# Kernel optimization log

Measured on AMD Instinct MI355X. Metric: run time of the kernel, lower is better.

The kernel has to match this reference:

```python
import jax, jax.numpy as jnp
import numpy as np

N_HEAD = 8
HIDDEN = 512
EPS_LN = 1e-3  # keras LayerNormalization default epsilon


def layernorm(x, gamma, beta, eps=EPS_LN):
    mu = jnp.mean(x, axis=-1, keepdims=True)
    var = jnp.mean((x - mu) ** 2, axis=-1, keepdims=True)
    return (x - mu) * jax.lax.rsqrt(var + eps) * gamma + beta


def setup_inputs() -> dict:
    key = jax.random.key(0)
    ks = jax.random.split(key, 10)
    bs, NE, F = 512, 128, HIDDEN
    x = jax.random.normal(ks[0], (bs, NE, F), dtype=jnp.float32)
    mask = (jax.random.uniform(ks[1], (bs, 1, NE)) < 0.85).astype(jnp.float32)
    # guarantee at least one live entity per row
    mask = mask.at[:, :, 0].set(1.0)
    s = 1.0 / np.sqrt(F)
    Wqk = jax.random.normal(ks[2], (F, 2 * HIDDEN), dtype=jnp.float32) * s
    bqk = jnp.zeros((2 * HIDDEN,), jnp.float32)
    Wv = jax.random.normal(ks[3], (F, HIDDEN), dtype=jnp.float32) * s
    bv = jnp.zeros((HIDDEN,), jnp.float32)
    Wmlp = jax.random.normal(ks[4], (F, HIDDEN), dtype=jnp.float32) * s
    bmlp = jnp.zeros((HIDDEN,), jnp.float32)
    g_pre = jnp.ones((F,), jnp.float32)
    b_pre = jnp.zeros((F,), jnp.float32)
    g_post = jnp.ones((F,), jnp.float32)
    b_post = jnp.zeros((F,), jnp.float32)
    return dict(x=x, mask=mask, Wqk=Wqk, bqk=bqk, Wv=Wv, bv=bv,
                Wmlp=Wmlp, bmlp=bmlp, g_pre=g_pre, b_pre=b_pre,
                g_post=g_post, b_post=b_post)


def reference(x, mask, Wqk, bqk, Wv, bv, Wmlp, bmlp, g_pre, b_pre, g_post, b_post):
    bs, NE, F = x.shape
    h, d = N_HEAD, HIDDEN // N_HEAD
    x4 = x[:, None]  # (bs, 1, NE, F)

    # pre-norm only feeds qkv projections; residual uses raw x4
    inp = layernorm(x4, g_pre, b_pre)

    qk = (inp @ Wqk + bqk).reshape(bs, 1, NE, h, d, 2)
    q, k = qk[..., 0], qk[..., 1]                       # (bs,1,NE,h,d)
    v = (inp @ Wv + bv).reshape(bs, 1, NE, h, d)

    logits = jnp.einsum('btnhd,btmhd->bthnm', q, k) / np.sqrt(d)  # (bs,1,h,NE,NE)

    m5 = mask[:, :, None, None, :]                      # (bs,1,1,1,NE)
    logits = logits - (1.0 - m5) * 1e10
    logits = logits - jnp.max(logits, axis=-1, keepdims=True)
    un = jnp.exp(logits) * m5
    p = un / (jnp.sum(un, axis=-1, keepdims=True) + 1e-10)
    p = p * m5

    att = jnp.einsum('bthnm,btmhd->btnhd', p, v).reshape(bs, 1, NE, HIDDEN)
    a = att @ Wmlp + bmlp                               # mlp_layer=1, no activation
    y = x4 + a                                          # residual
    y = layernorm(y, g_post, b_post)

    # masked average pooling over entities
    mE = mask[..., None]                                # (bs,1,NE,1)
    pooled = jnp.sum(y * mE, axis=-2) / (jnp.sum(mE, axis=-2) + 1e-5)  # (bs,1,F)
    return pooled.reshape(bs, F)
```

## Files before the change

### kernel.cpp

```cpp
#include <hip/hip_runtime.h>
#include <hip/hip_bf16.h>


typedef __bf16 bf16;
typedef __bf16 bf16x8 __attribute__((ext_vector_type(8)));
typedef __bf16 bf16x4 __attribute__((ext_vector_type(4)));
typedef float f32x4 __attribute__((ext_vector_type(4)));

__device__ __forceinline__ f32x4 mfma16(bf16x8 a, bf16x8 b, f32x4 c) {
    return __builtin_amdgcn_mfma_f32_16x16x32_bf16(a, b, c, 0, 0, 0);
}

typedef const unsigned int __attribute__((address_space(1)))* gptr_t;
typedef unsigned int __attribute__((address_space(3)))* lptr_t;
__device__ __forceinline__ void gld16(const void* g, void* l) {
    __builtin_amdgcn_global_load_lds((gptr_t)g, (lptr_t)l, 16, 0, 0);
}

#define SWZ(byteoff, row) ((byteoff) ^ (((row) & 7) << 4))


__global__ __launch_bounds__(256) void prep_split_kernel(
    const float* __restrict__ Wqk, const float* __restrict__ bqk,
    const float* __restrict__ Wv, const float* __restrict__ bv,
    const float* __restrict__ Wmlp,
    bf16* __restrict__ Wqkv_s, bf16* __restrict__ Wmlp_t, float* __restrict__ bQKV)
{
    int t = blockIdx.x * 256 + threadIdx.x;
    if (t < 524288) {
        int k = t >> 10, c = t & 1023;
        int h = c >> 7, w7 = c & 127, d = w7 >> 1, isK = w7 & 1;
        int n = isK * 512 + h * 64 + d;
        int tn = n >> 7, nc = n & 127, kc = k >> 6, kw = k & 63;
        Wqkv_s[((size_t)(tn * 8 + kc) * 128 + nc) * 64 + kw] = (bf16)Wqk[t];
    } else if (t < 786432) {
        int u = t - 524288;
        int k = u >> 9, c = u & 511;
        int n = 1024 + c;
        int tn = n >> 7, nc = n & 127, kc = k >> 6, kw = k & 63;
        Wqkv_s[((size_t)(tn * 8 + kc) * 128 + nc) * 64 + kw] = (bf16)Wv[u];
    } else if (t < 1048576) {
        int u = t - 786432;
        int k = u >> 9, c = u & 511;
        int tn = c >> 7, nc = c & 127, kc = k >> 6, kw = k & 63;
        Wmlp_t[((size_t)(tn * 8 + kc) * 128 + nc) * 64 + kw] = (bf16)Wmlp[u];
    } else if (t < 1050112) {
        int j = t - 1048576;
        int region = j >> 9, w9 = j & 511, h = w9 >> 6, d = w9 & 63;
        float v;
        if (region == 0)      v = bqk[h * 128 + d * 2];
        else if (region == 1) v = bqk[h * 128 + d * 2 + 1];
        else                  v = bv[h * 64 + d];
        bQKV[j] = v;
    }
}

__global__ __launch_bounds__(256) void ln_kernel(
    const float* __restrict__ x, const float* __restrict__ g,
    const float* __restrict__ b, bf16* __restrict__ inp)
{
    int row = blockIdx.x * 4 + (threadIdx.x >> 6);
    int lane = threadIdx.x & 63;
    int k0 = lane * 8;
    const float* xr = x + (size_t)row * 512 + k0;
    f32x4 a0 = *(const f32x4*)xr;
    f32x4 a1 = *(const f32x4*)(xr + 4);
    float s = 0.f, ss = 0.f;
#pragma unroll
    for (int i = 0; i < 4; i++) {
        s += a0[i] + a1[i];
        ss += a0[i] * a0[i] + a1[i] * a1[i];
    }
#pragma unroll
    for (int m = 1; m < 64; m <<= 1) {
        s  += __shfl_xor(s, m, 64);
        ss += __shfl_xor(ss, m, 64);
    }
    float mu = s * (1.f / 512.f);
    float rstd = rsqrtf(ss * (1.f / 512.f) - mu * mu + 1e-3f);
    f32x4 g0 = *(const f32x4*)(g + k0);
    f32x4 g1 = *(const f32x4*)(g + k0 + 4);
    f32x4 b0 = *(const f32x4*)(b + k0);
    f32x4 b1 = *(const f32x4*)(b + k0 + 4);
    bf16x8 ov;
#pragma unroll
    for (int i = 0; i < 4; i++) {
        ov[i]     = (bf16)((a0[i] - mu) * rstd * g0[i] + b0[i]);
        ov[i + 4] = (bf16)((a1[i] - mu) * rstd * g1[i] + b1[i]);
    }
    *(bf16x8*)(inp + (size_t)row * 512 + k0) = ov;
}

__global__ __launch_bounds__(256) void qkv_gemm_kernel(
    const bf16* __restrict__ inp, const bf16* __restrict__ Wqkv_s,
    const float* __restrict__ bQKV,
    bf16* __restrict__ q, bf16* __restrict__ kbuf, bf16* __restrict__ vt)
{
    __shared__ __align__(16) bf16 As[128 * 64];
    __shared__ __align__(16) bf16 Bs[128 * 64];
    const int bid = blockIdx.x;
    const int idx = (bid & 7) * 768 + (bid >> 3);
    const int tm = idx / 12, tn = idx % 12;
    const int tid = threadIdx.x;
    const int w = tid >> 6, l = tid & 63;
    const int wr = w >> 1, wc = w & 1;
    const int l15 = l & 15, l4 = l >> 4;

    const f32x4 fz = {0.f, 0.f, 0.f, 0.f};
    f32x4 acc[4][4];
#pragma unroll
    for (int m = 0; m < 4; m++)
#pragma unroll
        for (int n = 0; n < 4; n++) acc[m][n] = fz;

    const int arow = l >> 3;
    const int axc = ((l & 7) ^ arow) * 8;
    const bf16* Abase = inp + (size_t)(tm * 128) * 512;
    const int rsw = (l15 & 7) << 4;

    for (int kc = 0; kc < 8; kc++) {
#pragma unroll
        for (int i = 0; i < 4; i++) {
            int rg = (i * 4 + w) * 8;
            gld16(Abase + (size_t)(rg + arow) * 512 + kc * 64 + axc,
                  As + (i * 4 + w) * 512);
        }
        const bf16* Bbase = Wqkv_s + (size_t)(tn * 8 + kc) * 8192;
#pragma unroll
        for (int i = 0; i < 4; i++) {
            gld16(Bbase + (size_t)((i * 4 + w) * 8 + arow) * 64 + axc,
                  Bs + (i * 4 + w) * 512);
        }
        __syncthreads();
#pragma unroll
        for (int kk = 0; kk < 2; kk++) {
            const int kb = (kk * 64 + l4 * 16) ^ rsw;
            bf16x8 af[4], bfr[4];
#pragma unroll
            for (int m = 0; m < 4; m++)
                af[m] = *(const bf16x8*)((const char*)As + (wr * 64 + m * 16 + l15) * 128 + kb);
#pragma unroll
            for (int n = 0; n < 4; n++)
                bfr[n] = *(const bf16x8*)((const char*)Bs + (wc * 64 + n * 16 + l15) * 128 + kb);
#pragma unroll
            for (int m = 0; m < 4; m++)
#pragma unroll
                for (int n = 0; n < 4; n++)
                    acc[m][n] = mfma16(af[m], bfr[n], acc[m][n]);
        }
        __syncthreads();
    }

    const int colBase = tn * 128 + wc * 64;
    const int mrowBase = tm * 128 + wr * 64;
#pragma unroll
    for (int n = 0; n < 4; n++) {
        int col = colBase + n * 16 + l15;
        float bias = bQKV[col];
        int within = col & 511, hh = within >> 6, dd = within & 63;
#pragma unroll
        for (int m = 0; m < 4; m++) {
            int mr0 = mrowBase + m * 16 + l4 * 4;
            int bb = mr0 >> 7, e0 = mr0 & 127;
            size_t base = (size_t)(bb * 8 + hh) * 8192;
            if (tn < 4) {
#pragma unroll
                for (int r = 0; r < 4; r++)
                    q[base + (size_t)(e0 + r) * 64 + dd] = (bf16)(acc[m][n][r] + bias);
            } else if (tn < 8) {
#pragma unroll
                for (int r = 0; r < 4; r++) {
                    int e = e0 + r;
                    kbuf[base + (size_t)e * 64 + (dd ^ ((e & 7) << 3))] = (bf16)(acc[m][n][r] + bias);
                }
            } else {
                bf16x4 pk;
#pragma unroll
                for (int r = 0; r < 4; r++) pk[r] = (bf16)(acc[m][n][r] + bias);
                *(bf16x4*)(vt + base + (size_t)dd * 128 + (e0 ^ ((dd & 7) << 3))) = pk;
            }
        }
    }
}

__global__ __launch_bounds__(512) void attn_split_kernel(
    const bf16* __restrict__ q, const bf16* __restrict__ kbuf,
    const bf16* __restrict__ vt, const float* __restrict__ mask,
    bf16* __restrict__ att)
{
    __shared__ __align__(16) char Ks[128 * 128];
    __shared__ __align__(16) char VTs[64 * 256];
    __shared__ __align__(16) char Ps[128 * 256];
    __shared__ float mrow[128];

    const int bid = blockIdx.x;
    const int b = bid & 511, h = bid >> 9;
    const size_t bh = (size_t)(b * 8 + h);
    const int tid = threadIdx.x;
    const int w = tid >> 6, l = tid & 63;
    const int l15 = l & 15, l4 = l >> 4, R0 = w * 16;

    const bf16* kb = kbuf + bh * 8192;
    const bf16* vb = vt + bh * 8192;
#pragma unroll
    for (int i = 0; i < 2; i++) {
        gld16(kb + ((i * 8 + w) * 64 + l) * 8, (bf16*)Ks + (i * 8 + w) * 512);
        gld16(vb + ((i * 8 + w) * 64 + l) * 8, (bf16*)VTs + (i * 8 + w) * 512);
    }
    if (tid < 128) mrow[tid] = mask[b * 128 + tid];
    __syncthreads();

    const f32x4 fz = {0.f, 0.f, 0.f, 0.f};
    const bf16* qp = q + bh * 8192 + (size_t)(R0 + l15) * 64 + l4 * 8;
    bf16x8 af0 = *(const bf16x8*)(qp);
    bf16x8 af1 = *(const bf16x8*)(qp + 32);
    f32x4 accL[8];
#pragma unroll
    for (int n = 0; n < 8; n++) accL[n] = fz;
#pragma unroll
    for (int ks = 0; ks < 2; ks++) {
        bf16x8 af = ks ? af1 : af0;
        int k2 = (ks * 32 + l4 * 8) * 2;
#pragma unroll
        for (int nt = 0; nt < 8; nt++) {
            int krow = nt * 16 + l15;
            bf16x8 bfr = *(const bf16x8*)(Ks + krow * 128 + (k2 ^ ((krow & 7) << 4)));
            accL[nt] = mfma16(af, bfr, accL[nt]);
        }
    }
    float pv[32];
#pragma unroll
    for (int r = 0; r < 4; r++) {
        float mx = -1e30f;
#pragma unroll
        for (int nt = 0; nt < 8; nt++) {
            int colk = nt * 16 + l15;
            float v = accL[nt][r] * 0.125f - (1.0f - mrow[colk]) * 1e10f;
            pv[nt * 4 + r] = v;
            mx = fmaxf(mx, v);
        }
#pragma unroll
        for (int m = 1; m < 16; m <<= 1) mx = fmaxf(mx, __shfl_xor(mx, m, 64));
        float sum = 0.f;
#pragma unroll
        for (int nt = 0; nt < 8; nt++) {
            int colk = nt * 16 + l15;
            float e = __expf(pv[nt * 4 + r] - mx) * mrow[colk];
            pv[nt * 4 + r] = e;
            sum += e;
        }
#pragma unroll
        for (int m = 1; m < 16; m <<= 1) sum += __shfl_xor(sum, m, 64);
        float inv = 1.0f / (sum + 1e-10f);
        int prow = R0 + l4 * 4 + r;
#pragma unroll
        for (int nt = 0; nt < 8; nt++) {
            bf16 pb = (bf16)(pv[nt * 4 + r] * inv);
            *(bf16*)(Ps + prow * 256 + SWZ((nt * 16 + l15) * 2, prow)) = pb;
        }
    }
    __syncthreads();

    f32x4 accO[4];
#pragma unroll
    for (int n = 0; n < 4; n++) accO[n] = fz;
#pragma unroll
    for (int ks = 0; ks < 4; ks++) {
        int k2 = (ks * 32 + l4 * 8) * 2;
        int prow = R0 + l15;
        bf16x8 af = *(const bf16x8*)(Ps + prow * 256 + (k2 ^ ((prow & 7) << 4)));
#pragma unroll
        for (int nt = 0; nt < 4; nt++) {
            int d = nt * 16 + l15;
            bf16x8 bfr = *(const bf16x8*)(VTs + d * 256 + (k2 ^ ((d & 7) << 4)));
            accO[nt] = mfma16(af, bfr, accO[nt]);
        }
    }
    bf16* outp = att + (size_t)(b * 128) * 512 + h * 64;
#pragma unroll
    for (int nt = 0; nt < 4; nt++) {
        int d = nt * 16 + l15;
#pragma unroll
        for (int r = 0; r < 4; r++) {
            int e = R0 + l4 * 4 + r;
            outp[(size_t)e * 512 + d] = (bf16)accO[nt][r];
        }
    }
}

__global__ __launch_bounds__(256) void mlp_gemm_kernel(
    const bf16* __restrict__ att, const bf16* __restrict__ Wmlp_t,
    const float* __restrict__ bmlp, float* __restrict__ y)
{
    __shared__ __align__(16) bf16 As[128 * 64];
    __shared__ __align__(16) bf16 Bs[128 * 64];
    const int bid = blockIdx.x;
    const int idx = (bid & 7) * 256 + (bid >> 3);
    const int tm = idx >> 2, tn = idx & 3;
    const int tid = threadIdx.x;
    const int w = tid >> 6, l = tid & 63;
    const int wr = w >> 1, wc = w & 1;
    const int l15 = l & 15, l4 = l >> 4;

    const f32x4 fz = {0.f, 0.f, 0.f, 0.f};
    f32x4 acc[4][4];
#pragma unroll
    for (int m = 0; m < 4; m++)
#pragma unroll
        for (int n = 0; n < 4; n++) acc[m][n] = fz;

    const int arow = l >> 3;
    const int axc = ((l & 7) ^ arow) * 8;
    const bf16* Abase = att + (size_t)(tm * 128) * 512;
    const int rsw = (l15 & 7) << 4;

    for (int kc = 0; kc < 8; kc++) {
#pragma unroll
        for (int i = 0; i < 4; i++) {
            int rg = (i * 4 + w) * 8;
            gld16(Abase + (size_t)(rg + arow) * 512 + kc * 64 + axc,
                  As + (i * 4 + w) * 512);
        }
        const bf16* Bbase = Wmlp_t + (size_t)(tn * 8 + kc) * 8192;
#pragma unroll
        for (int i = 0; i < 4; i++) {
            gld16(Bbase + (size_t)((i * 4 + w) * 8 + arow) * 64 + axc,
                  Bs + (i * 4 + w) * 512);
        }
        __syncthreads();
#pragma unroll
        for (int kk = 0; kk < 2; kk++) {
            const int kb = (kk * 64 + l4 * 16) ^ rsw;
            bf16x8 af[4], bfr[4];
#pragma unroll
            for (int m = 0; m < 4; m++)
                af[m] = *(const bf16x8*)((const char*)As + (wr * 64 + m * 16 + l15) * 128 + kb);
#pragma unroll
            for (int n = 0; n < 4; n++)
                bfr[n] = *(const bf16x8*)((const char*)Bs + (wc * 64 + n * 16 + l15) * 128 + kb);
#pragma unroll
            for (int m = 0; m < 4; m++)
#pragma unroll
                for (int n = 0; n < 4; n++)
                    acc[m][n] = mfma16(af[m], bfr[n], acc[m][n]);
        }
        __syncthreads();
    }

    const int colBase = tn * 128 + wc * 64;
    const int mrowBase = tm * 128 + wr * 64;
#pragma unroll
    for (int n = 0; n < 4; n++) {
        int col = colBase + n * 16 + l15;
        float bias = bmlp[col];
#pragma unroll
        for (int m = 0; m < 4; m++) {
            int row0 = mrowBase + m * 16 + l4 * 4;
#pragma unroll
            for (int r = 0; r < 4; r++)
                y[(size_t)(row0 + r) * 512 + col] = acc[m][n][r] + bias;
        }
    }
}

__global__ __launch_bounds__(512) void pool_kernel(
    const float* __restrict__ y, const float* __restrict__ x,
    const float* __restrict__ mask, const float* __restrict__ gpost,
    const float* __restrict__ bpost, float* __restrict__ out)
{
    __shared__ float partial[8][512];
    __shared__ float mrow[128];
    __shared__ float msum_s;

    const int b = blockIdx.x;
    const int tid = threadIdx.x;
    const int w = tid >> 6, l = tid & 63;
    const int k0 = l * 8;

    if (tid < 128) mrow[tid] = mask[b * 128 + tid];
    __syncthreads();
    if (w == 0) {
        float v = mrow[l] + mrow[64 + l];
#pragma unroll
        for (int m = 1; m < 64; m <<= 1) v += __shfl_xor(v, m, 64);
        if (l == 0) msum_s = v;
    }

    f32x4 g0 = *(const f32x4*)(gpost + k0);
    f32x4 g1 = *(const f32x4*)(gpost + k0 + 4);
    f32x4 b0 = *(const f32x4*)(bpost + k0);
    f32x4 b1 = *(const f32x4*)(bpost + k0 + 4);

    f32x4 a0 = {0.f, 0.f, 0.f, 0.f}, a1 = {0.f, 0.f, 0.f, 0.f};
    for (int i = 0; i < 16; i++) {
        int row = w * 16 + i;
        const float* yr = y + ((size_t)(b * 128 + row)) * 512 + k0;
        const float* xr = x + ((size_t)(b * 128 + row)) * 512 + k0;
        f32x4 v0 = *(const f32x4*)yr + *(const f32x4*)xr;
        f32x4 v1 = *(const f32x4*)(yr + 4) + *(const f32x4*)(xr + 4);
        float s = 0.f, ss = 0.f;
#pragma unroll
        for (int j = 0; j < 4; j++) {
            s += v0[j] + v1[j];
            ss += v0[j] * v0[j] + v1[j] * v1[j];
        }
#pragma unroll
        for (int m = 1; m < 64; m <<= 1) {
            s  += __shfl_xor(s, m, 64);
            ss += __shfl_xor(ss, m, 64);
        }
        float mu = s * (1.f / 512.f);
        float rstd = rsqrtf(ss * (1.f / 512.f) - mu * mu + 1e-3f);
        float mr = mrow[row];
#pragma unroll
        for (int j = 0; j < 4; j++) {
            a0[j] += ((v0[j] - mu) * rstd * g0[j] + b0[j]) * mr;
            a1[j] += ((v1[j] - mu) * rstd * g1[j] + b1[j]) * mr;
        }
    }
#pragma unroll
    for (int j = 0; j < 4; j++) {
        partial[w][k0 + j]     = a0[j];
        partial[w][k0 + 4 + j] = a1[j];
    }
    __syncthreads();
    float t = 0.f;
#pragma unroll
    for (int ww = 0; ww < 8; ww++) t += partial[ww][tid];
    out[(size_t)b * 512 + tid] = t / (msum_s + 1e-5f);
}

__global__ __launch_bounds__(256) void prep_kernel(
    const float* __restrict__ Wqk, const float* __restrict__ bqk,
    const float* __restrict__ Wv, const float* __restrict__ bv,
    const float* __restrict__ Wmlp,
    bf16* __restrict__ Wqkv_t, bf16* __restrict__ Wmlp_t, float* __restrict__ bQKV)
{
    int t = blockIdx.x * 256 + threadIdx.x;
    const int NQKV = 8 * 192 * 512;
    if (t < NQKV) {
        int h = t / (192 * 512);
        int rem = t - h * (192 * 512);
        int n = rem >> 9;
        int k = rem & 511;
        float v;
        if (n < 64)       v = Wqk[k * 1024 + h * 128 + n * 2];
        else if (n < 128) v = Wqk[k * 1024 + h * 128 + (n - 64) * 2 + 1];
        else              v = Wv[k * 512 + h * 64 + (n - 128)];
        Wqkv_t[t] = (bf16)v;
    } else {
        int u = t - NQKV;
        if (u < 512 * 512) {
            int col = u >> 9, k = u & 511;
            Wmlp_t[u] = (bf16)Wmlp[k * 512 + col];
        } else {
            int j = u - 512 * 512;
            if (j < 1536) {
                int h = j / 192, n = j - h * 192;
                float v;
                if (n < 64)       v = bqk[h * 128 + n * 2];
                else if (n < 128) v = bqk[h * 128 + (n - 64) * 2 + 1];
                else              v = bv[h * 64 + (n - 128)];
                bQKV[j] = v;
            }
        }
    }
}

__global__ __launch_bounds__(512) void attn_kernel(
    const bf16* __restrict__ inp, const float* __restrict__ mask,
    const bf16* __restrict__ Wqkv_t, const float* __restrict__ bQKV,
    bf16* __restrict__ att)
{
    __shared__ __align__(16) char Qs[128 * 128];
    __shared__ __align__(16) char Ks[128 * 128];
    __shared__ __align__(16) char VTs[64 * 256];
    __shared__ __align__(16) char Ps[128 * 256];
    __shared__ float mrow[128];

    const int bid = blockIdx.x;
    const int b = bid & 511;
    const int h = bid >> 9;
    const int tid = threadIdx.x;
    const int w = tid >> 6, l = tid & 63;
    const int l15 = l & 15, l4 = l >> 4;
    const int R0 = w * 16;

    if (tid < 128) mrow[tid] = mask[b * 128 + tid];

    const bf16* A  = inp + (size_t)(b * 128) * 512;
    const bf16* Wh = Wqkv_t + (size_t)h * 192 * 512;
    const f32x4 fz = {0.f, 0.f, 0.f, 0.f};

    f32x4 acc[12];
#pragma unroll
    for (int n = 0; n < 12; n++) acc[n] = fz;
    const bf16* aptr = A + (size_t)(R0 + l15) * 512 + l4 * 8;
#pragma unroll 4
    for (int ks = 0; ks < 16; ks++) {
        bf16x8 af = *(const bf16x8*)(aptr + ks * 32);
#pragma unroll
        for (int n = 0; n < 12; n++) {
            bf16x8 bfr = *(const bf16x8*)(Wh + (size_t)(n * 16 + l15) * 512 + ks * 32 + l4 * 8);
            acc[n] = mfma16(af, bfr, acc[n]);
        }
    }
#pragma unroll
    for (int n = 0; n < 12; n++) {
        int col = n * 16 + l15;
        float bias = bQKV[h * 192 + col];
#pragma unroll
        for (int r = 0; r < 4; r++) {
            int row = R0 + l4 * 4 + r;
            bf16 val = (bf16)(acc[n][r] + bias);
            if (n < 4) {
                *(bf16*)(Qs + row * 128 + SWZ(col * 2, row)) = val;
            } else if (n < 8) {
                *(bf16*)(Ks + row * 128 + SWZ((col - 64) * 2, row)) = val;
            } else {
                int d = col - 128;
                *(bf16*)(VTs + d * 256 + SWZ(row * 2, d)) = val;
            }
        }
    }
    __syncthreads();

    f32x4 accL[8];
#pragma unroll
    for (int n = 0; n < 8; n++) accL[n] = fz;
#pragma unroll
    for (int ks = 0; ks < 2; ks++) {
        int k = ks * 32 + l4 * 8;
        int qrow = R0 + l15;
        bf16x8 af = *(const bf16x8*)(Qs + qrow * 128 + SWZ(k * 2, qrow));
#pragma unroll
        for (int nt = 0; nt < 8; nt++) {
            int krow = nt * 16 + l15;
            bf16x8 bfr = *(const bf16x8*)(Ks + krow * 128 + SWZ(k * 2, krow));
            accL[nt] = mfma16(af, bfr, accL[nt]);
        }
    }
    float pv[32];
#pragma unroll
    for (int r = 0; r < 4; r++) {
        float mx = -1e30f;
#pragma unroll
        for (int nt = 0; nt < 8; nt++) {
            int colk = nt * 16 + l15;
            float v = accL[nt][r] * 0.125f - (1.0f - mrow[colk]) * 1e10f;
            pv[nt * 4 + r] = v;
            mx = fmaxf(mx, v);
        }
#pragma unroll
        for (int m = 1; m < 16; m <<= 1) mx = fmaxf(mx, __shfl_xor(mx, m, 64));
        float sum = 0.f;
#pragma unroll
        for (int nt = 0; nt < 8; nt++) {
            int colk = nt * 16 + l15;
            float e = __expf(pv[nt * 4 + r] - mx) * mrow[colk];
            pv[nt * 4 + r] = e;
            sum += e;
        }
#pragma unroll
        for (int m = 1; m < 16; m <<= 1) sum += __shfl_xor(sum, m, 64);
        float inv = 1.0f / (sum + 1e-10f);
        int prow = R0 + l4 * 4 + r;
#pragma unroll
        for (int nt = 0; nt < 8; nt++) {
            bf16 pb = (bf16)(pv[nt * 4 + r] * inv);
            *(bf16*)(Ps + prow * 256 + SWZ((nt * 16 + l15) * 2, prow)) = pb;
        }
    }
    __syncthreads();

    f32x4 accO[4];
#pragma unroll
    for (int n = 0; n < 4; n++) accO[n] = fz;
#pragma unroll
    for (int ks = 0; ks < 4; ks++) {
        int k = ks * 32 + l4 * 8;
        int prow = R0 + l15;
        bf16x8 af = *(const bf16x8*)(Ps + prow * 256 + SWZ(k * 2, prow));
#pragma unroll
        for (int nt = 0; nt < 4; nt++) {
            int d = nt * 16 + l15;
            bf16x8 bfr = *(const bf16x8*)(VTs + d * 256 + SWZ(k * 2, d));
            accO[nt] = mfma16(af, bfr, accO[nt]);
        }
    }
    bf16* outp = att + (size_t)(b * 128) * 512 + h * 64;
#pragma unroll
    for (int nt = 0; nt < 4; nt++) {
        int d = nt * 16 + l15;
#pragma unroll
        for (int r = 0; r < 4; r++) {
            int e = R0 + l4 * 4 + r;
            outp[(size_t)e * 512 + d] = (bf16)accO[nt][r];
        }
    }
}

__global__ __launch_bounds__(512) void mlp_kernel(
    const bf16* __restrict__ att, const bf16* __restrict__ Wmlp_t,
    const float* __restrict__ bmlp, const float* __restrict__ x,
    const float* __restrict__ mask, const float* __restrict__ gpost,
    const float* __restrict__ bpost, float* __restrict__ out)
{
    __shared__ float pool[512];
    __shared__ float gb[1024];
    __shared__ float mrow[128];
    __shared__ float msum_s;

    const int b = blockIdx.x;
    const int tid = threadIdx.x;
    const int w = tid >> 6, l = tid & 63;
    const int l15 = l & 15, l4 = l >> 4;
    const int R0 = w * 16;

    pool[tid] = 0.f;
    gb[tid] = gpost[tid];
    gb[512 + tid] = bpost[tid];
    if (tid < 128) mrow[tid] = mask[b * 128 + tid];
    __syncthreads();
    if (w == 0) {
        float v = mrow[l] + mrow[64 + l];
#pragma unroll
        for (int m = 1; m < 64; m <<= 1) v += __shfl_xor(v, m, 64);
        if (l == 0) msum_s = v;
    }

    const f32x4 fz = {0.f, 0.f, 0.f, 0.f};
    f32x4 acc[32];
#pragma unroll
    for (int n = 0; n < 32; n++) acc[n] = fz;
    const bf16* Ab = att + (size_t)(b * 128 + R0 + l15) * 512 + l4 * 8;
#pragma unroll 2
    for (int ks = 0; ks < 16; ks++) {
        bf16x8 af = *(const bf16x8*)(Ab + ks * 32);
#pragma unroll
        for (int nt = 0; nt < 32; nt++) {
            bf16x8 bfr = *(const bf16x8*)(Wmlp_t + (size_t)(nt * 16 + l15) * 512 + ks * 32 + l4 * 8);
            acc[nt] = mfma16(af, bfr, acc[nt]);
        }
    }
#pragma unroll
    for (int nt = 0; nt < 32; nt++) {
        int col = nt * 16 + l15;
        float bb = bmlp[col];
#pragma unroll
        for (int r = 0; r < 4; r++) {
            int row = R0 + l4 * 4 + r;
            acc[nt][r] = acc[nt][r] + bb + x[((size_t)b * 128 + row) * 512 + col];
        }
    }
    float mu[4], rs[4];
#pragma unroll
    for (int r = 0; r < 4; r++) {
        float s = 0.f, ss = 0.f;
#pragma unroll
        for (int nt = 0; nt < 32; nt++) {
            float v = acc[nt][r];
            s += v; ss += v * v;
        }
#pragma unroll
        for (int m = 1; m < 16; m <<= 1) {
            s  += __shfl_xor(s, m, 64);
            ss += __shfl_xor(ss, m, 64);
        }
        float m_ = s * (1.f / 512.f);
        mu[r] = m_;
        rs[r] = rsqrtf(ss * (1.f / 512.f) - m_ * m_ + 1e-3f);
    }
#pragma unroll
    for (int nt = 0; nt < 32; nt++) {
        int col = nt * 16 + l15;
        float g = gb[col], bb = gb[512 + col];
        float s = 0.f;
#pragma unroll
        for (int r = 0; r < 4; r++) {
            int row = R0 + l4 * 4 + r;
            float y = (acc[nt][r] - mu[r]) * rs[r] * g + bb;
            s += y * mrow[row];
        }
        atomicAdd(&pool[col], s);
    }
    __syncthreads();
    out[(size_t)b * 512 + tid] = pool[tid] / (msum_s + 1e-5f);
}

extern "C" void kernel_launch(void* const* d_in, const int* in_sizes, int n_in,
                              void* d_out, int out_size, void* d_ws, size_t ws_size,
                              hipStream_t stream)
{
    const float* x     = (const float*)d_in[0];
    const float* mask  = (const float*)d_in[1];
    const float* Wqk   = (const float*)d_in[2];
    const float* bqk   = (const float*)d_in[3];
    const float* Wv    = (const float*)d_in[4];
    const float* bv    = (const float*)d_in[5];
    const float* Wmlp  = (const float*)d_in[6];
    const float* bmlp  = (const float*)d_in[7];
    const float* gpre  = (const float*)d_in[8];
    const float* bpre  = (const float*)d_in[9];
    const float* gpost = (const float*)d_in[10];
    const float* bpost = (const float*)d_in[11];
    float* out = (float*)d_out;
    char* ws = (char*)d_ws;

    const size_t NEED_SPLIT = 270538752;
    if (ws_size >= NEED_SPLIT) {
        bf16*  q      = (bf16*)ws;
        bf16*  kbuf   = (bf16*)(ws + (size_t)67108864);
        bf16*  vt     = (bf16*)(ws + (size_t)134217728);
        bf16*  inp    = (bf16*)(ws + (size_t)201326592);
        bf16*  att    = inp;
        float* y      = (float*)ws;
        bf16*  Wqkv_s = (bf16*)(ws + (size_t)268435456);
        bf16*  Wmlp_t = (bf16*)(ws + (size_t)270008320);
        float* bQKV   = (float*)(ws + (size_t)270532608);

        prep_split_kernel<<<4103, 256, 0, stream>>>(Wqk, bqk, Wv, bv, Wmlp, Wqkv_s, Wmlp_t, bQKV);
        ln_kernel<<<16384, 256, 0, stream>>>(x, gpre, bpre, inp);
        qkv_gemm_kernel<<<6144, 256, 0, stream>>>(inp, Wqkv_s, bQKV, q, kbuf, vt);
        attn_split_kernel<<<4096, 512, 0, stream>>>(q, kbuf, vt, mask, att);
        mlp_gemm_kernel<<<2048, 256, 0, stream>>>(att, Wmlp_t, bmlp, y);
        pool_kernel<<<512, 512, 0, stream>>>(y, x, mask, gpost, bpost, out);
    } else {
        bf16*  inp    = (bf16*)ws;
        bf16*  att    = (bf16*)(ws + 67108864);
        bf16*  Wqkv_t = (bf16*)(ws + 134217728);
        bf16*  Wmlp_t = (bf16*)(ws + 134217728 + 1572864);
        float* bQKV   = (float*)(ws + 134217728 + 1572864 + 524288);

        prep_kernel<<<4103, 256, 0, stream>>>(Wqk, bqk, Wv, bv, Wmlp, Wqkv_t, Wmlp_t, bQKV);
        ln_kernel<<<16384, 256, 0, stream>>>(x, gpre, bpre, inp);
        attn_kernel<<<4096, 512, 0, stream>>>(inp, mask, Wqkv_t, bQKV, att);
        mlp_kernel<<<512, 512, 0, stream>>>(att, Wmlp_t, bmlp, x, mask, gpost, bpost, out);
    }
}
```

Baseline: 556.7 us.

## Loop heads per block with double-buffered K/V and register-resident softmax

The attention kernel now launches one block per batch element, looping over all 8 heads and prefetching the next head's K and V^T into a second LDS buffer while the current head computes. The QK^T MFMA is transposed (K as the A operand), so each lane's softmax row lives in registers and needs only two cross-lane shuffles. The P tile is repacked through lane shuffles instead of an LDS round trip. This removes the P shared buffer and one barrier per head, but cuts the grid from 4096 to 512 blocks, which may underfill the GPU's compute units, and it serializes the heads inside each block.

Result: no change. 563.9 us (+1.3%).

```diff
diff --git a/kernel.cpp b/kernel.cpp
--- a/kernel.cpp
+++ b/kernel.cpp
@@ -6,6 +6,7 @@
 typedef __bf16 bf16x8 __attribute__((ext_vector_type(8)));
 typedef __bf16 bf16x4 __attribute__((ext_vector_type(4)));
 typedef float f32x4 __attribute__((ext_vector_type(4)));
+typedef unsigned u32x4 __attribute__((ext_vector_type(4)));
 
 __device__ __forceinline__ f32x4 mfma16(bf16x8 a, bf16x8 b, f32x4 c) {
     return __builtin_amdgcn_mfma_f32_16x16x32_bf16(a, b, c, 0, 0, 0);
@@ -15,6 +16,12 @@
 typedef unsigned int __attribute__((address_space(3)))* lptr_t;
 __device__ __forceinline__ void gld16(const void* g, void* l) {
     __builtin_amdgcn_global_load_lds((gptr_t)g, (lptr_t)l, 16, 0, 0);
+}
+
+__device__ __forceinline__ unsigned pack2(float lo, float hi) {
+    unsigned short a = __builtin_bit_cast(unsigned short, (bf16)lo);
+    unsigned short b = __builtin_bit_cast(unsigned short, (bf16)hi);
+    return (unsigned)a | ((unsigned)b << 16);
 }
 
 #define SWZ(byteoff, row) ((byteoff) ^ (((row) & 7) << 4))
@@ -183,108 +190,137 @@
     }
 }
 
-__global__ __launch_bounds__(512) void attn_split_kernel(
+__global__ __launch_bounds__(512) void attn_fused_kernel(
     const bf16* __restrict__ q, const bf16* __restrict__ kbuf,
     const bf16* __restrict__ vt, const float* __restrict__ mask,
     bf16* __restrict__ att)
 {
-    __shared__ __align__(16) char Ks[128 * 128];
-    __shared__ __align__(16) char VTs[64 * 256];
-    __shared__ __align__(16) char Ps[128 * 256];
+    __shared__ __align__(16) char Ks[2][128 * 128];
+    __shared__ __align__(16) char VTs[2][64 * 256];
     __shared__ float mrow[128];
 
-    const int bid = blockIdx.x;
-    const int b = bid & 511, h = bid >> 9;
-    const size_t bh = (size_t)(b * 8 + h);
+    const int b = blockIdx.x;
+    const size_t bh0 = (size_t)b * 8;
     const int tid = threadIdx.x;
     const int w = tid >> 6, l = tid & 63;
     const int l15 = l & 15, l4 = l >> 4, R0 = w * 16;
 
-    const bf16* kb = kbuf + bh * 8192;
-    const bf16* vb = vt + bh * 8192;
-#pragma unroll
-    for (int i = 0; i < 2; i++) {
-        gld16(kb + ((i * 8 + w) * 64 + l) * 8, (bf16*)Ks + (i * 8 + w) * 512);
-        gld16(vb + ((i * 8 + w) * 64 + l) * 8, (bf16*)VTs + (i * 8 + w) * 512);
-    }
     if (tid < 128) mrow[tid] = mask[b * 128 + tid];
+
+    {
+        const bf16* kb = kbuf + bh0 * 8192;
+        const bf16* vb = vt + bh0 * 8192;
+#pragma unroll
+        for (int i = 0; i < 2; i++) {
+            gld16(kb + ((i * 8 + w) * 64 + l) * 8, (bf16*)Ks[0] + (i * 8 + w) * 512);
+            gld16(vb + ((i * 8 + w) * 64 + l) * 8, (bf16*)VTs[0] + (i * 8 + w) * 512);
+        }
+    }
+    const bf16* qp0 = q + bh0 * 8192 + (size_t)(R0 + l15) * 64 + l4 * 8;
+    bf16x8 afn0 = *(const bf16x8*)(qp0);
+    bf16x8 afn1 = *(const bf16x8*)(qp0 + 32);
     __syncthreads();
 
     const f32x4 fz = {0.f, 0.f, 0.f, 0.f};
-    const bf16* qp = q + bh * 8192 + (size_t)(R0 + l15) * 64 + l4 * 8;
-    bf16x8 af0 = *(const bf16x8*)(qp);
-    bf16x8 af1 = *(const bf16x8*)(qp + 32);
-    f32x4 accL[8];
-#pragma unroll
-    for (int n = 0; n < 8; n++) accL[n] = fz;
-#pragma unroll
-    for (int ks = 0; ks < 2; ks++) {
-        bf16x8 af = ks ? af1 : af0;
-        int k2 = (ks * 32 + l4 * 8) * 2;
-#pragma unroll
-        for (int nt = 0; nt < 8; nt++) {
-            int krow = nt * 16 + l15;
-            bf16x8 bfr = *(const bf16x8*)(Ks + krow * 128 + (k2 ^ ((krow & 7) << 4)));
-            accL[nt] = mfma16(af, bfr, accL[nt]);
-        }
-    }
-    float pv[32];
-#pragma unroll
-    for (int r = 0; r < 4; r++) {
+    for (int h = 0; h < 8; h++) {
+        const int cur = h & 1;
+        bf16x8 af0 = afn0, af1 = afn1;
+        if (h < 7) {
+            const bf16* kb = kbuf + (bh0 + h + 1) * 8192;
+            const bf16* vb = vt + (bh0 + h + 1) * 8192;
+#pragma unroll
+            for (int i = 0; i < 2; i++) {
+                gld16(kb + ((i * 8 + w) * 64 + l) * 8, (bf16*)Ks[cur ^ 1] + (i * 8 + w) * 512);
+                gld16(vb + ((i * 8 + w) * 64 + l) * 8, (bf16*)VTs[cur ^ 1] + (i * 8 + w) * 512);
+            }
+            const bf16* qp = q + (bh0 + h + 1) * 8192 + (size_t)(R0 + l15) * 64 + l4 * 8;
+            afn0 = *(const bf16x8*)(qp);
+            afn1 = *(const bf16x8*)(qp + 32);
+        }
+
+        f32x4 accL[8];
+#pragma unroll
+        for (int n = 0; n < 8; n++) accL[n] = fz;
+#pragma unroll
+        for (int ks = 0; ks < 2; ks++) {
+            bf16x8 bq = ks ? af1 : af0;
+            const int k2 = ks * 64 + l4 * 16;
+#pragma unroll
+            for (int nt = 0; nt < 8; nt++) {
+                const int krow = nt * 16 + l15;
+                bf16x8 kf = *(const bf16x8*)(Ks[cur] + krow * 128 + (k2 ^ ((krow & 7) << 4)));
+                accL[nt] = mfma16(kf, bq, accL[nt]);
+            }
+        }
+
         float mx = -1e30f;
 #pragma unroll
-        for (int nt = 0; nt < 8; nt++) {
-            int colk = nt * 16 + l15;
-            float v = accL[nt][r] * 0.125f - (1.0f - mrow[colk]) * 1e10f;
-            pv[nt * 4 + r] = v;
-            mx = fmaxf(mx, v);
-        }
-#pragma unroll
-        for (int m = 1; m < 16; m <<= 1) mx = fmaxf(mx, __shfl_xor(mx, m, 64));
+        for (int nt = 0; nt < 8; nt++)
+#pragma unroll
+            for (int r = 0; r < 4; r++) {
+                float mk = mrow[nt * 16 + l4 * 4 + r];
+                float v = accL[nt][r] * 0.125f - (1.0f - mk) * 1e10f;
+                accL[nt][r] = v;
+                mx = fmaxf(mx, v);
+            }
+        mx = fmaxf(mx, __shfl_xor(mx, 16, 64));
+        mx = fmaxf(mx, __shfl_xor(mx, 32, 64));
         float sum = 0.f;
 #pragma unroll
-        for (int nt = 0; nt < 8; nt++) {
-            int colk = nt * 16 + l15;
-            float e = __expf(pv[nt * 4 + r] - mx) * mrow[colk];
-            pv[nt * 4 + r] = e;
-            sum += e;
-        }
-#pragma unroll
-        for (int m = 1; m < 16; m <<= 1) sum += __shfl_xor(sum, m, 64);
-        float inv = 1.0f / (sum + 1e-10f);
-        int prow = R0 + l4 * 4 + r;
-#pragma unroll
-        for (int nt = 0; nt < 8; nt++) {
-            bf16 pb = (bf16)(pv[nt * 4 + r] * inv);
-            *(bf16*)(Ps + prow * 256 + SWZ((nt * 16 + l15) * 2, prow)) = pb;
-        }
-    }
-    __syncthreads();
-
-    f32x4 accO[4];
-#pragma unroll
-    for (int n = 0; n < 4; n++) accO[n] = fz;
-#pragma unroll
-    for (int ks = 0; ks < 4; ks++) {
-        int k2 = (ks * 32 + l4 * 8) * 2;
-        int prow = R0 + l15;
-        bf16x8 af = *(const bf16x8*)(Ps + prow * 256 + (k2 ^ ((prow & 7) << 4)));
+        for (int nt = 0; nt < 8; nt++)
+#pragma unroll
+            for (int r = 0; r < 4; r++) {
+                float mk = mrow[nt * 16 + l4 * 4 + r];
+                float e = __expf(accL[nt][r] - mx) * mk;
+                accL[nt][r] = e;
+                sum += e;
+            }
+        sum += __shfl_xor(sum, 16, 64);
+        sum += __shfl_xor(sum, 32, 64);
+        const float inv = 1.0f / (sum + 1e-10f);
+
+        unsigned pk[8][2];
+#pragma unroll
+        for (int nt = 0; nt < 8; nt++)
+#pragma unroll
+            for (int qq = 0; qq < 2; qq++)
+                pk[nt][qq] = pack2(accL[nt][2 * qq] * inv, accL[nt][2 * qq + 1] * inv);
+
+        f32x4 accO[4];
+#pragma unroll
+        for (int n = 0; n < 4; n++) accO[n] = fz;
+        const int glo = l15 + ((l4 & 1) << 5);
+#pragma unroll
+        for (int ks = 0; ks < 4; ks++) {
+            u32x4 pa4;
+#pragma unroll
+            for (int p = 0; p < 4; p++) {
+                int srcl = glo + ((p >> 1) << 4);
+                unsigned va = (unsigned)__shfl((int)pk[2 * ks][p & 1], srcl, 64);
+                unsigned vb = (unsigned)__shfl((int)pk[2 * ks + 1][p & 1], srcl, 64);
+                pa4[p] = (l4 & 2) ? vb : va;
+            }
+            bf16x8 pa = __builtin_bit_cast(bf16x8, pa4);
+            const int e2 = ks * 64 + l4 * 16;
+#pragma unroll
+            for (int nt = 0; nt < 4; nt++) {
+                const int d = nt * 16 + l15;
+                bf16x8 vf = *(const bf16x8*)(VTs[cur] + d * 256 + (e2 ^ ((d & 7) << 4)));
+                accO[nt] = mfma16(pa, vf, accO[nt]);
+            }
+        }
+
+        bf16* outp = att + (size_t)(b * 128) * 512 + h * 64;
 #pragma unroll
         for (int nt = 0; nt < 4; nt++) {
-            int d = nt * 16 + l15;
-            bf16x8 bfr = *(const bf16x8*)(VTs + d * 256 + (k2 ^ ((d & 7) << 4)));
-            accO[nt] = mfma16(af, bfr, accO[nt]);
-        }
-    }
-    bf16* outp = att + (size_t)(b * 128) * 512 + h * 64;
-#pragma unroll
-    for (int nt = 0; nt < 4; nt++) {
-        int d = nt * 16 + l15;
-#pragma unroll
-        for (int r = 0; r < 4; r++) {
-            int e = R0 + l4 * 4 + r;
-            outp[(size_t)e * 512 + d] = (bf16)accO[nt][r];
-        }
+            const int d = nt * 16 + l15;
+#pragma unroll
+            for (int r = 0; r < 4; r++) {
+                const int e = R0 + l4 * 4 + r;
+                outp[(size_t)e * 512 + d] = (bf16)accO[nt][r];
+            }
+        }
+        __syncthreads();
     }
 }
 
@@ -722,7 +758,7 @@
         prep_split_kernel<<<4103, 256, 0, stream>>>(Wqk, bqk, Wv, bv, Wmlp, Wqkv_s, Wmlp_t, bQKV);
         ln_kernel<<<16384, 256, 0, stream>>>(x, gpre, bpre, inp);
         qkv_gemm_kernel<<<6144, 256, 0, stream>>>(inp, Wqkv_s, bQKV, q, kbuf, vt);
-        attn_split_kernel<<<4096, 512, 0, stream>>>(q, kbuf, vt, mask, att);
+        attn_fused_kernel<<<512, 512, 0, stream>>>(q, kbuf, vt, mask, att);
         mlp_gemm_kernel<<<2048, 256, 0, stream>>>(att, Wmlp_t, bmlp, y);
         pool_kernel<<<512, 512, 0, stream>>>(y, x, mask, gpost, bpost, out);
     } else {
```
